# Performance work log

Hardware: AMD Instinct MI355X
Metric: run time of the kernel (lower is better)

The kernel has to match this reference:

```python
import jax, jax.numpy as jnp
from jax import lax
import numpy as np

BN_EPS = 1e-3  # keras BatchNormalization default epsilon


def setup_inputs() -> dict:
    key = jax.random.key(0)
    ks = jax.random.split(key, 7)
    B, T, Feat, Ch = 64, 4096, 32, 16
    kh, kw, F = 3, 32, 16
    return {
        "x": jax.random.normal(ks[0], (B, T, Feat, Ch), dtype=jnp.float32),
        "kernel": jax.random.normal(ks[1], (kh, kw, 1, F), dtype=jnp.float32) * 0.05,
        "bias": jax.random.normal(ks[2], (F,), dtype=jnp.float32) * 0.05,
        "gamma": jax.random.uniform(ks[3], (T,), dtype=jnp.float32),
        "beta": jax.random.normal(ks[4], (T,), dtype=jnp.float32) * 0.1,
        "moving_mean": jax.random.normal(ks[5], (T,), dtype=jnp.float32) * 0.1,
        "moving_var": jax.random.uniform(ks[6], (T,), dtype=jnp.float32),
    }


def reference(x, kernel, bias, gamma, beta, moving_mean, moving_var):
    # x: (B, T, Feat, Ch). Original loops over T, feeding (B, Ch, Feat, 1) to one
    # shared Conv2D; we batch all T timesteps into one conv call (same math).
    B, T, Feat, Ch = x.shape
    kh, kw, _, F = kernel.shape
    inp = jnp.transpose(x, (0, 1, 3, 2)).reshape(B * T, Ch, Feat, 1)  # (B*T, H=Ch, W=Feat, 1)
    y = lax.conv_general_dilated(
        inp, kernel, window_strides=(1, 1), padding="VALID",
        dimension_numbers=("NHWC", "HWIO", "NHWC"),
    ) + bias  # (B*T, Hp, Wp, F)
    Hp, Wp = y.shape[1], y.shape[2]  # Hp = Ch-kh+1, Wp = Feat-kw+1 (=1 here)
    # per-timestep transpose [0,1,3,2] -> (B, Hp, F, Wp), then concat over T on last axis
    y = y.reshape(B, T, Hp, Wp, F)
    y = jnp.transpose(y, (0, 2, 4, 1, 3)).reshape(B, Hp, F, T * Wp)
    # Dropout: identity at inference. BatchNormalization(axis=-1) in inference mode:
    y = (y - moving_mean) * (gamma / jnp.sqrt(moving_var + BN_EPS)) + beta
    y = jax.nn.relu(y)
    # not last layer: transpose [0,3,1,2] -> (B, T, Hp, F)
    return jnp.transpose(y, (0, 3, 1, 2))
```

## Files before the change

kernel.cpp:

```cpp
#include <hip/hip_runtime.h>
#include <hip/hip_bf16.h>


typedef __attribute__((ext_vector_type(8))) short bf16x8;
typedef __attribute__((ext_vector_type(4))) float f32x4;

#define NBT 32
#define XSTRIDE 40
#define XTILE (18 * XSTRIDE + 8)
#define WSTRIDE 104

__device__ __forceinline__ unsigned short f2bf(float f) {
    unsigned u = __builtin_bit_cast(unsigned, f);
    return (unsigned short)((u + 0x7fffu + ((u >> 16) & 1u)) >> 16);
}
__device__ __forceinline__ unsigned pack2(float a, float b) {
    return (unsigned)f2bf(a) | ((unsigned)f2bf(b) << 16);
}

__global__ __launch_bounds__(256) void tccnn_mfma(
    const float* __restrict__ x,
    const float* __restrict__ kern,
    const float* __restrict__ bias,
    const float* __restrict__ gamma,
    const float* __restrict__ beta,
    const float* __restrict__ mmean,
    const float* __restrict__ mvar,
    float* __restrict__ out)
{
    __shared__ __align__(16) unsigned short xs[NBT * XTILE];
    __shared__ __align__(16) unsigned short wsh[16 * WSTRIDE];

    const int tid = threadIdx.x;
    const long bt0 = (long)blockIdx.x * NBT;

    for (int idx = tid; idx < 1536; idx += 256) {
        int ij = idx >> 4, f = idx & 15;
        wsh[f * WSTRIDE + ij] = f2bf(kern[idx]);
    }

    #pragma unroll
    for (int v = 0; v < 4; ++v) {
        int U = v * 256 + tid;
        int btl = U >> 5, u = U & 31;
        int cu = u & 3, ju = u >> 2;
        const float4* src = (const float4*)(x + (bt0 + btl) * 512 + ju * 4 * 16 + cu * 4);
        float4 r0 = src[0];
        float4 r1 = src[4];
        float4 r2 = src[8];
        float4 r3 = src[12];
        unsigned short* dst = &xs[btl * XTILE + ju * 4];
        *(uint2*)&dst[(cu * 4 + 0) * XSTRIDE] =
            make_uint2(pack2(r0.x, r1.x), pack2(r2.x, r3.x));
        *(uint2*)&dst[(cu * 4 + 1) * XSTRIDE] =
            make_uint2(pack2(r0.y, r1.y), pack2(r2.y, r3.y));
        *(uint2*)&dst[(cu * 4 + 2) * XSTRIDE] =
            make_uint2(pack2(r0.z, r1.z), pack2(r2.z, r3.z));
        *(uint2*)&dst[(cu * 4 + 3) * XSTRIDE] =
            make_uint2(pack2(r0.w, r1.w), pack2(r2.w, r3.w));
    }
    __syncthreads();

    const int lane = tid & 63;
    const int wv = tid >> 6;
    const int f = lane & 15;
    const int g = lane >> 4;

    bf16x8 bfr0 = *(const bf16x8*)&wsh[f * WSTRIDE + 0 * 32 + g * 8];
    bf16x8 bfr1 = *(const bf16x8*)&wsh[f * WSTRIDE + 1 * 32 + g * 8];
    bf16x8 bfr2 = *(const bf16x8*)&wsh[f * WSTRIDE + 2 * 32 + g * 8];
    const float bsf = bias[f];

    #pragma unroll 4
    for (int q = 0; q < 8; ++q) {
        const int btl = wv * 8 + q;
        const unsigned short* xt = &xs[btl * XTILE];
        bf16x8 a0 = *(const bf16x8*)&xt[(f + 0) * XSTRIDE + g * 8];
        bf16x8 a1 = *(const bf16x8*)&xt[(f + 1) * XSTRIDE + g * 8];
        bf16x8 a2 = *(const bf16x8*)&xt[(f + 2) * XSTRIDE + g * 8];

        f32x4 acc = {0.f, 0.f, 0.f, 0.f};
        acc = __builtin_amdgcn_mfma_f32_16x16x32_bf16(a0, bfr0, acc, 0, 0, 0);
        acc = __builtin_amdgcn_mfma_f32_16x16x32_bf16(a1, bfr1, acc, 0, 0, 0);
        acc = __builtin_amdgcn_mfma_f32_16x16x32_bf16(a2, bfr2, acc, 0, 0, 0);

        const long bt = bt0 + btl;
        const int t = (int)(bt & 4095);
        const float sc = gamma[t] * rsqrtf(mvar[t] + 1e-3f);
        const float sh = beta[t] - mmean[t] * sc;
        float* ob = out + bt * 224 + f;
        #pragma unroll
        for (int r = 0; r < 4; ++r) {
            int row = g * 4 + r;
            if (row < 14)
                ob[row * 16] = fmaxf((acc[r] + bsf) * sc + sh, 0.f);
        }
    }
}

extern "C" void kernel_launch(void* const* d_in, const int* in_sizes, int n_in,
                              void* d_out, int out_size, void* d_ws, size_t ws_size,
                              hipStream_t stream) {
    const float* x     = (const float*)d_in[0];
    const float* kern  = (const float*)d_in[1];
    const float* bias  = (const float*)d_in[2];
    const float* gamma = (const float*)d_in[3];
    const float* beta  = (const float*)d_in[4];
    const float* mmean = (const float*)d_in[5];
    const float* mvar  = (const float*)d_in[6];
    float* out = (float*)d_out;

    const int n_bt = 64 * 4096;
    const int blocks = n_bt / NBT;
    tccnn_mfma<<<blocks, 256, 0, stream>>>(x, kern, bias, gamma, beta,
                                           mmean, mvar, out);
}
```

Before: 151.6 us.

## Swap MFMA operands for vectorized float4 stores and halve tile per block

```diff
diff --git a/kernel.cpp b/kernel.cpp
--- a/kernel.cpp
+++ b/kernel.cpp
@@ -5,7 +5,7 @@
 typedef __attribute__((ext_vector_type(8))) short bf16x8;
 typedef __attribute__((ext_vector_type(4))) float f32x4;
 
-#define NBT 32
+#define NBT 16
 #define XSTRIDE 40
 #define XTILE (18 * XSTRIDE + 8)
 #define WSTRIDE 104
@@ -34,66 +34,67 @@
     const int tid = threadIdx.x;
     const long bt0 = (long)blockIdx.x * NBT;
 
-    for (int idx = tid; idx < 1536; idx += 256) {
+    #pragma unroll
+    for (int v = 0; v < 6; ++v) {
+        int idx = v * 256 + tid;
         int ij = idx >> 4, f = idx & 15;
         wsh[f * WSTRIDE + ij] = f2bf(kern[idx]);
     }
 
-    #pragma unroll
-    for (int v = 0; v < 4; ++v) {
-        int U = v * 256 + tid;
-        int btl = U >> 5, u = U & 31;
+    {
+        int U = tid;
+        int btl = U >> 4, u = U & 15;
         int cu = u & 3, ju = u >> 2;
-        const float4* src = (const float4*)(x + (bt0 + btl) * 512 + ju * 4 * 16 + cu * 4);
-        float4 r0 = src[0];
-        float4 r1 = src[4];
-        float4 r2 = src[8];
-        float4 r3 = src[12];
-        unsigned short* dst = &xs[btl * XTILE + ju * 4];
-        *(uint2*)&dst[(cu * 4 + 0) * XSTRIDE] =
-            make_uint2(pack2(r0.x, r1.x), pack2(r2.x, r3.x));
-        *(uint2*)&dst[(cu * 4 + 1) * XSTRIDE] =
-            make_uint2(pack2(r0.y, r1.y), pack2(r2.y, r3.y));
-        *(uint2*)&dst[(cu * 4 + 2) * XSTRIDE] =
-            make_uint2(pack2(r0.z, r1.z), pack2(r2.z, r3.z));
-        *(uint2*)&dst[(cu * 4 + 3) * XSTRIDE] =
-            make_uint2(pack2(r0.w, r1.w), pack2(r2.w, r3.w));
+        const float4* src = (const float4*)(x + (bt0 + btl) * 512 + ju * 128 + cu * 4);
+        float4 r0 = src[0],  r1 = src[4],  r2 = src[8],  r3 = src[12];
+        float4 r4 = src[16], r5 = src[20], r6 = src[24], r7 = src[28];
+        unsigned short* dst = &xs[btl * XTILE + ju * 8];
+        *(uint4*)&dst[(cu * 4 + 0) * XSTRIDE] = make_uint4(
+            pack2(r0.x, r1.x), pack2(r2.x, r3.x), pack2(r4.x, r5.x), pack2(r6.x, r7.x));
+        *(uint4*)&dst[(cu * 4 + 1) * XSTRIDE] = make_uint4(
+            pack2(r0.y, r1.y), pack2(r2.y, r3.y), pack2(r4.y, r5.y), pack2(r6.y, r7.y));
+        *(uint4*)&dst[(cu * 4 + 2) * XSTRIDE] = make_uint4(
+            pack2(r0.z, r1.z), pack2(r2.z, r3.z), pack2(r4.z, r5.z), pack2(r6.z, r7.z));
+        *(uint4*)&dst[(cu * 4 + 3) * XSTRIDE] = make_uint4(
+            pack2(r0.w, r1.w), pack2(r2.w, r3.w), pack2(r4.w, r5.w), pack2(r6.w, r7.w));
     }
     __syncthreads();
 
     const int lane = tid & 63;
     const int wv = tid >> 6;
-    const int f = lane & 15;
+    const int hp = lane & 15;
     const int g = lane >> 4;
 
-    bf16x8 bfr0 = *(const bf16x8*)&wsh[f * WSTRIDE + 0 * 32 + g * 8];
-    bf16x8 bfr1 = *(const bf16x8*)&wsh[f * WSTRIDE + 1 * 32 + g * 8];
-    bf16x8 bfr2 = *(const bf16x8*)&wsh[f * WSTRIDE + 2 * 32 + g * 8];
-    const float bsf = bias[f];
+    bf16x8 bfr0 = *(const bf16x8*)&wsh[hp * WSTRIDE + 0 * 32 + g * 8];
+    bf16x8 bfr1 = *(const bf16x8*)&wsh[hp * WSTRIDE + 1 * 32 + g * 8];
+    bf16x8 bfr2 = *(const bf16x8*)&wsh[hp * WSTRIDE + 2 * 32 + g * 8];
+    const float4 b4 = *(const float4*)&bias[g * 4];
 
-    #pragma unroll 4
-    for (int q = 0; q < 8; ++q) {
-        const int btl = wv * 8 + q;
+    #pragma unroll
+    for (int q = 0; q < 4; ++q) {
+        const int btl = wv * 4 + q;
         const unsigned short* xt = &xs[btl * XTILE];
-        bf16x8 a0 = *(const bf16x8*)&xt[(f + 0) * XSTRIDE + g * 8];
-        bf16x8 a1 = *(const bf16x8*)&xt[(f + 1) * XSTRIDE + g * 8];
-        bf16x8 a2 = *(const bf16x8*)&xt[(f + 2) * XSTRIDE + g * 8];
+        bf16x8 a0 = *(const bf16x8*)&xt[(hp + 0) * XSTRIDE + g * 8];
+        bf16x8 a1 = *(const bf16x8*)&xt[(hp + 1) * XSTRIDE + g * 8];
+        bf16x8 a2 = *(const bf16x8*)&xt[(hp + 2) * XSTRIDE + g * 8];
 
         f32x4 acc = {0.f, 0.f, 0.f, 0.f};
-        acc = __builtin_amdgcn_mfma_f32_16x16x32_bf16(a0, bfr0, acc, 0, 0, 0);
-        acc = __builtin_amdgcn_mfma_f32_16x16x32_bf16(a1, bfr1, acc, 0, 0, 0);
-        acc = __builtin_amdgcn_mfma_f32_16x16x32_bf16(a2, bfr2, acc, 0, 0, 0);
+        acc = __builtin_amdgcn_mfma_f32_16x16x32_bf16(bfr0, a0, acc, 0, 0, 0);
+        acc = __builtin_amdgcn_mfma_f32_16x16x32_bf16(bfr1, a1, acc, 0, 0, 0);
+        acc = __builtin_amdgcn_mfma_f32_16x16x32_bf16(bfr2, a2, acc, 0, 0, 0);
 
         const long bt = bt0 + btl;
         const int t = (int)(bt & 4095);
         const float sc = gamma[t] * rsqrtf(mvar[t] + 1e-3f);
         const float sh = beta[t] - mmean[t] * sc;
-        float* ob = out + bt * 224 + f;
-        #pragma unroll
-        for (int r = 0; r < 4; ++r) {
-            int row = g * 4 + r;
-            if (row < 14)
-                ob[row * 16] = fmaxf((acc[r] + bsf) * sc + sh, 0.f);
+
+        if (hp < 14) {
+            float4 y;
+            y.x = fmaxf((acc[0] + b4.x) * sc + sh, 0.f);
+            y.y = fmaxf((acc[1] + b4.y) * sc + sh, 0.f);
+            y.z = fmaxf((acc[2] + b4.z) * sc + sh, 0.f);
+            y.w = fmaxf((acc[3] + b4.w) * sc + sh, 0.f);
+            *(float4*)(out + bt * 224 + hp * 16 + g * 4) = y;
         }
     }
 }
```

Measured after the change: 140.8 us. 7.1% less time.
